# Kernel optimization log

Measured on AMD Instinct MI355X. Metric: run time of the kernel, lower is better.

Reference implementation:

```python
import jax, jax.numpy as jnp
import numpy as np

N = 20000   # total_nodes
B = 8       # batch of graphs
E = 320000  # edges per graph (avg degree 16)
FD = 128    # node feature dim
D = 64      # latent_dim
H = 128     # mlp_hidden
MAX_LV = 2  # message-passing levels


def setup_inputs() -> dict:
    key = jax.random.key(0)
    ks = jax.random.split(key, 16)
    def gn(k, shape, fan_in):
        return jax.random.normal(k, shape, dtype=jnp.float32) / np.sqrt(fan_in)
    edges_src = jax.random.randint(ks[0], (B, E), 0, N)
    edges_dst = jax.random.randint(ks[1], (B, E), 0, N)
    # row-normalized adjacency weights: w = 1/deg(dst)  (GraphNormTool mean norm)
    deg = jax.vmap(lambda d: jnp.zeros((N,), jnp.float32).at[d].add(1.0))(edges_dst)
    edge_w = 1.0 / jnp.take_along_axis(deg, edges_dst, axis=1)
    return {
        "node_features": jax.random.normal(ks[2], (N, FD), dtype=jnp.float32),
        "w_n2l": gn(ks[3], (FD, D), FD),
        "bias_n2l": jnp.zeros((D,), jnp.float32),
        "bias_picked": gn(ks[4], (1, D), D),
        "conv_W": gn(ks[5], (D, D), D),
        "conv_b": jnp.zeros((D,), jnp.float32),
        "lin1_W": gn(ks[6], (2 * D, H), 2 * D),
        "lin1_b": jnp.zeros((H,), jnp.float32),
        "lout_W": gn(ks[7], (H, D), H),
        "lout_b": jnp.zeros((D,), jnp.float32),
        "edge_w": edge_w,
        "edges_src": edges_src,
        "edges_dst": edges_dst,
        "target_nodes": jax.random.randint(ks[8], (B,), 0, N),
        "picked_nodes": jax.random.randint(ks[9], (B,), 0, N),
    }


def reference(node_features, w_n2l, bias_n2l, bias_picked, conv_W, conv_b,
              lin1_W, lin1_b, lout_W, lout_b, edge_w,
              edges_src, edges_dst, target_nodes, picked_nodes):
    # shared input linear: [N, D]
    base = node_features @ w_n2l + bias_n2l

    def per_graph(src, dst, w, tgt, picked):
        # inject picked-node bias (sparse one-hot spmm in original)
        input_message = base.at[picked].add(bias_picked[0])
        h = jax.nn.relu(input_message)
        for _ in range(MAX_LV):
            # n2npool = adj @ h  (sparse spmm via gather + segment_sum)
            pooled = jax.ops.segment_sum(h[src] * w[:, None], dst, num_segments=N)
            h = jax.nn.relu(pooled @ conv_W + conv_b + input_message)
        target_embed = h[tgt]                      # [D]
        graph_embed = jnp.mean(h, axis=0)          # [D]
        e = jnp.concatenate([h, jnp.broadcast_to(graph_embed, (N, D))], axis=1)
        e = jax.nn.relu(e @ lin1_W + lin1_b)       # [N, H]
        raw = e @ lout_W + lout_b                  # [N, D]
        return raw @ target_embed                  # bilin_q: [N]

    q = jax.vmap(per_graph)(edges_src, edges_dst, edge_w, target_nodes, picked_nodes)
    return q  # [B, N] per-node Q values per graph
```

## Files before the change

kernel.cpp:

```cpp
#include <hip/hip_runtime.h>
#include <hip/hip_bf16.h>
#include <hip/hip_fp16.h>

#define Nn 20000
#define NR 20001
#define Bg 8
#define Eg 320000
#define FDim 128
#define Dd 64
#define Hh 128
#define NCH 16
#define CHE (Eg / NCH)

typedef _Float16 v2h __attribute__((ext_vector_type(2)));
typedef unsigned short u16;

__device__ __forceinline__ float bcastf(float v, int l) {
  return __int_as_float(__builtin_amdgcn_readlane(__float_as_int(v), l));
}
__device__ __forceinline__ int bcasti(int v, int l) {
  return __builtin_amdgcn_readlane(v, l);
}
__device__ __forceinline__ v2h u2h2(unsigned u) { return __builtin_bit_cast(v2h, u); }
__device__ __forceinline__ unsigned h22u(__half2 h) { return __builtin_bit_cast(unsigned, h); }
__device__ __forceinline__ float fdot2f(v2h a, v2h b, float c) {
  return __builtin_amdgcn_fdot2(a, b, c, false);
}

__global__ __launch_bounds__(256) void k_base(const float* __restrict__ x,
                                              const float* __restrict__ W,
                                              const float* __restrict__ b,
                                              float* __restrict__ base,
                                              __half* __restrict__ b16,
                                              __half* __restrict__ b16p) {
  __shared__ float Wl[FDim * Dd];
  int t = threadIdx.x;
  for (int i = t; i < FDim * Dd; i += 256) Wl[i] = W[i];
  __syncthreads();
  int wv = t >> 6, lane = t & 63;
  float bias = b[lane];
  for (int row = blockIdx.x * 4 + wv; row < NR; row += gridDim.x * 4) {
    if (row == Nn) {
      b16[(size_t)row * Dd + lane] = __float2half(0.f);
      continue;
    }
    float x0 = x[row * FDim + lane];
    float x1 = x[row * FDim + 64 + lane];
    float acc = bias;
#pragma unroll
    for (int k = 0; k < 64; ++k) acc = fmaf(bcastf(x0, k), Wl[k * Dd + lane], acc);
#pragma unroll
    for (int k = 0; k < 64; ++k) acc = fmaf(bcastf(x1, k), Wl[(64 + k) * Dd + lane], acc);
    base[row * Dd + lane] = acc;
    b16[row * Dd + lane] = __float2half(fmaxf(acc, 0.f));
    b16p[row * Dd + lane] = __float2half(acc);
  }
}

__global__ __launch_bounds__(1024) void k_hist(const int* __restrict__ dst,
                                               int* __restrict__ hpart) {
  __shared__ int lh[Nn];
  int g = blockIdx.x & 7;
  int c = blockIdx.x >> 3;
  for (int i = threadIdx.x; i < Nn; i += 1024) lh[i] = 0;
  __syncthreads();
  const int* dp = dst + (size_t)g * Eg + c * CHE;
  for (int e4 = threadIdx.x * 4; e4 < CHE; e4 += 4096) {
    int4 d4 = *(const int4*)(dp + e4);
    atomicAdd(&lh[d4.x], 1);
    atomicAdd(&lh[d4.y], 1);
    atomicAdd(&lh[d4.z], 1);
    atomicAdd(&lh[d4.w], 1);
  }
  __syncthreads();
  int* out = hpart + (size_t)(g * NCH + c) * Nn;
  for (int i = threadIdx.x; i < Nn; i += 1024) out[i] = lh[i];
}

__global__ __launch_bounds__(1024) void k_scan(int* __restrict__ hpart,
                                               int* __restrict__ deg,
                                               int* __restrict__ offs,
                                               __half* __restrict__ hA) {
  int g = blockIdx.x;
  if (threadIdx.x < Dd)
    hA[((size_t)g * NR + Nn) * Dd + threadIdx.x] = __float2half(0.f);
  int* hp = hpart + (size_t)g * NCH * Nn;
  int* dp = deg + g * Nn;
  int* op = offs + g * Nn;
  __shared__ int wsum[16];
  __shared__ int carrysh;
  if (threadIdx.x == 0) carrysh = 0;
  int lane = threadIdx.x & 63, wv = threadIdx.x >> 6;
  __syncthreads();
  for (int b0 = 0; b0 < Nn; b0 += 4096) {
    int gidx = b0 + threadIdx.x * 4;
    bool ok = (gidx < Nn);
    int4 s = make_int4(0, 0, 0, 0);
    if (ok) {
#pragma unroll
      for (int c = 0; c < NCH; ++c) {
        int4 v = *(const int4*)(hp + (size_t)c * Nn + gidx);
        s.x += v.x; s.y += v.y; s.z += v.z; s.w += v.w;
      }
      *(int4*)(dp + gidx) = s;
    }
    int s0 = s.x, s1 = s0 + s.y, s2 = s1 + s.z, s3 = s2 + s.w;
    int incl = s3;
#pragma unroll
    for (int off = 1; off < 64; off <<= 1) {
      int y = __shfl_up(incl, off, 64);
      if (lane >= off) incl += y;
    }
    if (lane == 63) wsum[wv] = incl;
    __syncthreads();
    if (threadIdx.x < 16) {
      int w = wsum[threadIdx.x];
      int wincl = w;
#pragma unroll
      for (int off = 1; off < 16; off <<= 1) {
        int y = __shfl_up(wincl, off, 64);
        if (lane >= off) wincl += y;
      }
      wsum[threadIdx.x] = wincl - w;
    }
    __syncthreads();
    int cc = carrysh;
    int excl = cc + wsum[wv] + incl - s3;
    if (ok) {
      int4 o;
      o.x = excl; o.y = excl + s0; o.z = excl + s1; o.w = excl + s2;
      *(int4*)(op + gidx) = o;
      int4 run = o;
#pragma unroll
      for (int c = 0; c < NCH; ++c) {
        int4 v = *(const int4*)(hp + (size_t)c * Nn + gidx);
        *(int4*)(hp + (size_t)c * Nn + gidx) = run;
        run.x += v.x; run.y += v.y; run.z += v.z; run.w += v.w;
      }
    }
    __syncthreads();
    if (threadIdx.x == 1023) carrysh = cc + wsum[15] + __shfl(incl, 63, 64);
    __syncthreads();
  }
}

__global__ __launch_bounds__(1024) void k_scatter(const int* __restrict__ src,
                                                  const int* __restrict__ dst,
                                                  const int* __restrict__ basep,
                                                  u16* __restrict__ ssrc) {
  __shared__ int lc[Nn];
  int g = blockIdx.x & 7;
  int c = blockIdx.x >> 3;
  for (int i = threadIdx.x; i < Nn; i += 1024) lc[i] = 0;
  __syncthreads();
  const int* dp = dst + (size_t)g * Eg + c * CHE;
  const int* sp_in = src + (size_t)g * Eg + c * CHE;
  const int* bp = basep + (size_t)(g * NCH + c) * Nn;
  u16* out = ssrc + (size_t)g * Eg;
  for (int e4 = threadIdx.x * 4; e4 < CHE; e4 += 4096) {
    int4 d4 = *(const int4*)(dp + e4);
    int4 s4 = *(const int4*)(sp_in + e4);
    int r0 = atomicAdd(&lc[d4.x], 1); out[bp[d4.x] + r0] = (u16)s4.x;
    int r1 = atomicAdd(&lc[d4.y], 1); out[bp[d4.y] + r1] = (u16)s4.y;
    int r2 = atomicAdd(&lc[d4.z], 1); out[bp[d4.z] + r2] = (u16)s4.z;
    int r3 = atomicAdd(&lc[d4.w], 1); out[bp[d4.w] + r3] = (u16)s4.w;
  }
}

template <bool LV1>
__global__ __launch_bounds__(256, 4) void k_level(
    const __half* __restrict__ gsrc,
    __half* __restrict__ hout,
    const float* __restrict__ base,
    const __half* __restrict__ b16p,
    const float* __restrict__ convW, const float* __restrict__ convb,
    const float* __restrict__ biasp, const int* __restrict__ picked,
    const int* __restrict__ deg, const int* __restrict__ offs,
    const u16* __restrict__ ssrc, float* __restrict__ gsum) {
  int t = threadIdx.x;
  int wv = t >> 6, lane = t & 63;
  unsigned wc[32];
#pragma unroll
  for (int d2 = 0; d2 < 32; ++d2)
    wc[d2] = h22u(__floats2half2_rn(convW[(2 * d2) * Dd + lane],
                                    (convW[(2 * d2 + 1) * Dd + lane])));
#pragma unroll
  for (int d2 = 0; d2 < 32; ++d2) asm volatile("" : "+v"(wc[d2]));
  float cb = convb[lane];
  float bp = biasp[lane];
  int g = blockIdx.x & 7;
  int lb = blockIdx.x >> 3;
  int pstride = (gridDim.x >> 3) * 4;
  int pick = picked[g];
  int gN = g * Nn;
  const u16* sp = ssrc + (size_t)g * Eg;
  const __half* hsrc = LV1 ? gsrc : (gsrc + (size_t)g * NR * Dd);
  __half* outp = LV1 ? (hout + (size_t)g * NR * Dd) : (hout + (size_t)g * Nn * Dd);
  float delta = 0.f;
  if (LV1) {
    float db = base[(size_t)pick * Dd + lane];
    float d16 = __half2float(__float2half(fmaxf(db, 0.f)));
    delta = fmaxf(db + bp, 0.f) - d16;
  }
  float gs = 0.f;

  for (int p = lb * 4 + wv; p < Nn / 2; p += pstride) {
    int i0 = p * 2, i1 = i0 + 1;
    int2 dg2 = *(const int2*)&deg[gN + i0];
    int d0 = dg2.x, dtot = d0 + dg2.y;
    int beg0 = offs[gN + i0];

    float a0 = 0.f, aT = 0.f;
    if (dtot <= 64) {
      int svm = Nn;
      if (lane < dtot) svm = (int)sp[beg0 + lane];
      if (LV1) {
        unsigned long long pm = __ballot(svm == pick);
        unsigned long long m0 = (d0 >= 64) ? ~0ull : ((1ull << d0) - 1ull);
        a0 += (float)__popcll(pm & m0) * delta;
        aT += (float)__popcll(pm) * delta;
      }
      int nch = (dtot + 7) >> 3;
      for (int c = 0; c < nch; ++c) {
        int j = c * 8;
        int s0 = bcasti(svm, j + 0), s1 = bcasti(svm, j + 1);
        int s2 = bcasti(svm, j + 2), s3 = bcasti(svm, j + 3);
        int s4 = bcasti(svm, j + 4), s5 = bcasti(svm, j + 5);
        int s6 = bcasti(svm, j + 6), s7 = bcasti(svm, j + 7);
        float v0 = __half2float(hsrc[((unsigned)s0 << 6) + lane]);
        float v1 = __half2float(hsrc[((unsigned)s1 << 6) + lane]);
        float v2 = __half2float(hsrc[((unsigned)s2 << 6) + lane]);
        float v3 = __half2float(hsrc[((unsigned)s3 << 6) + lane]);
        float v4 = __half2float(hsrc[((unsigned)s4 << 6) + lane]);
        float v5 = __half2float(hsrc[((unsigned)s5 << 6) + lane]);
        float v6 = __half2float(hsrc[((unsigned)s6 << 6) + lane]);
        float v7 = __half2float(hsrc[((unsigned)s7 << 6) + lane]);
        float cs = ((v0 + v1) + (v2 + v3)) + ((v4 + v5) + (v6 + v7));
        aT += cs;
        if (j + 8 <= d0) {
          a0 += cs;
        } else if (j < d0) {
          int r = d0 - j;
          float pfx = (r > 0 ? v0 : 0.f) + (r > 1 ? v1 : 0.f) + (r > 2 ? v2 : 0.f) +
                      (r > 3 ? v3 : 0.f) + (r > 4 ? v4 : 0.f) + (r > 5 ? v5 : 0.f) +
                      (r > 6 ? v6 : 0.f);
          a0 += pfx;
        }
      }
    } else {
      int c0cnt = 0, cTcnt = 0;
      int end0 = beg0 + d0, end1 = beg0 + dtot;
      for (int e = beg0; e < end0; ++e) {
        int s = (int)sp[e];
        if (LV1) c0cnt += (s == pick);
        a0 += __half2float(hsrc[((unsigned)s << 6) + lane]);
      }
      aT = a0;
      for (int e = end0; e < end1; ++e) {
        int s = (int)sp[e];
        if (LV1) cTcnt += (s == pick);
        aT += __half2float(hsrc[((unsigned)s << 6) + lane]);
      }
      if (LV1) {
        a0 += (float)c0cnt * delta;
        aT += (float)(cTcnt + c0cnt) * delta;
      }
    }
    float a1 = aT - a0;
    float acc0 = a0 * (d0 ? 1.0f / (float)d0 : 0.f);
    float acc1 = a1 * (dg2.y ? 1.0f / (float)dg2.y : 0.f);

    unsigned p0 = h22u(__floats2half2_rn(acc0, __shfl_down(acc0, 1, 64)));
    unsigned p1 = h22u(__floats2half2_rn(acc1, __shfl_down(acc1, 1, 64)));

    float o0a = __half2float(b16p[(size_t)i0 * Dd + lane]) + cb, o0b = 0.f;
    float o1a = __half2float(b16p[(size_t)i1 * Dd + lane]) + cb, o1b = 0.f;
    if (i0 == pick) o0a += bp;
    if (i1 == pick) o1a += bp;
#pragma unroll
    for (int d2 = 0; d2 < 32; d2 += 2) {
      v2h m00 = u2h2(bcasti(p0, 2 * d2)),     m01 = u2h2(bcasti(p0, 2 * d2 + 2));
      v2h m10 = u2h2(bcasti(p1, 2 * d2)),     m11 = u2h2(bcasti(p1, 2 * d2 + 2));
      o0a = fdot2f(m00, u2h2(wc[d2]), o0a);
      o0b = fdot2f(m01, u2h2(wc[d2 + 1]), o0b);
      o1a = fdot2f(m10, u2h2(wc[d2]), o1a);
      o1b = fdot2f(m11, u2h2(wc[d2 + 1]), o1b);
    }
    float out0 = fmaxf(o0a + o0b, 0.f);
    float out1 = fmaxf(o1a + o1b, 0.f);
    outp[(size_t)i0 * Dd + lane] = __float2half(out0);
    outp[(size_t)i1 * Dd + lane] = __float2half(out1);
    if (!LV1) gs += out0 + out1;
  }
  if (!LV1) atomicAdd(&gsum[g * Dd + lane], gs);
}

__global__ __launch_bounds__(128) void k_prep(
    const __half* __restrict__ h2, const float* __restrict__ gsum,
    const int* __restrict__ tgt, const float* __restrict__ lin1W,
    const float* __restrict__ lin1b, const float* __restrict__ loutW,
    const float* __restrict__ loutb, float* __restrict__ cvec,
    float* __restrict__ uvec, float* __restrict__ cscal) {
  int g = blockIdx.x;
  int k = threadIdx.x;
  __shared__ float tv[Dd], ge[Dd];
  if (k < Dd) {
    tv[k] = __half2float(h2[(size_t)g * Nn * Dd + (size_t)tgt[g] * Dd + k]);
    ge[k] = gsum[g * Dd + k] * (1.0f / Nn);
  }
  __syncthreads();
  float cv = lin1b[k];
#pragma unroll 8
  for (int d = 0; d < Dd; ++d) cv = fmaf(ge[d], lin1W[(Dd + d) * Hh + k], cv);
  cvec[g * Hh + k] = cv;
  float uu = 0.f;
#pragma unroll 8
  for (int j = 0; j < Dd; ++j) uu = fmaf(loutW[k * Dd + j], tv[j], uu);
  uvec[g * Hh + k] = uu;
  if (k == 0) {
    float c = 0.f;
    for (int j = 0; j < Dd; ++j) c += loutb[j] * tv[j];
    cscal[g] = c;
  }
}

__global__ __launch_bounds__(256) void k_final(
    const __half* __restrict__ h2, const float* __restrict__ lin1W,
    const float* __restrict__ cvec, const float* __restrict__ uvec,
    const float* __restrict__ cscal, float* __restrict__ out) {
  __shared__ unsigned Wl2[32 * Hh];
  int t = threadIdx.x;
  for (int i = t; i < 32 * Hh; i += 256) {
    int d2 = i >> 7, c = i & 127;
    Wl2[i] = h22u(__floats2half2_rn(lin1W[(2 * d2) * Hh + c],
                                    lin1W[(2 * d2 + 1) * Hh + c]));
  }
  __syncthreads();
  int wv = t >> 6, lane = t & 63;
  int lr = lane & 31, hi = lane >> 5;
  int tot = Bg * Nn / 4;
  for (int p = blockIdx.x * 4 + wv; p < tot; p += gridDim.x * 4) {
    int row0 = p * 4;
    int g = row0 / Nn;
    int i0 = row0 - g * Nn;
    const __half2* hb = (const __half2*)(h2 + (size_t)g * Nn * Dd);
    unsigned ra = h22u(hb[(size_t)(i0 + hi) * 32 + lr]);
    unsigned rb = h22u(hb[(size_t)(i0 + 2 + hi) * 32 + lr]);
    float c0 = cvec[g * Hh + lane], c1 = cvec[g * Hh + 64 + lane];
    float u0 = uvec[g * Hh + lane], u1 = uvec[g * Hh + 64 + lane];
    float za0 = c0, za1 = c1, zb0 = c0, zb1 = c1;
    float zc0 = c0, zc1 = c1, zd0 = c0, zd1 = c1;
#pragma unroll
    for (int d2 = 0; d2 < 32; ++d2) {
      v2h w0 = u2h2(Wl2[d2 * Hh + lane]);
      v2h w1 = u2h2(Wl2[d2 * Hh + 64 + lane]);
      v2h a0 = u2h2(bcasti(ra, d2)), a1 = u2h2(bcasti(ra, 32 + d2));
      v2h b0 = u2h2(bcasti(rb, d2)), b1 = u2h2(bcasti(rb, 32 + d2));
      za0 = fdot2f(a0, w0, za0);  za1 = fdot2f(a0, w1, za1);
      zb0 = fdot2f(a1, w0, zb0);  zb1 = fdot2f(a1, w1, zb1);
      zc0 = fdot2f(b0, w0, zc0);  zc1 = fdot2f(b0, w1, zc1);
      zd0 = fdot2f(b1, w0, zd0);  zd1 = fdot2f(b1, w1, zd1);
    }
    float s0 = fmaxf(za0, 0.f) * u0 + fmaxf(za1, 0.f) * u1;
    float s1 = fmaxf(zb0, 0.f) * u0 + fmaxf(zb1, 0.f) * u1;
    float s2 = fmaxf(zc0, 0.f) * u0 + fmaxf(zc1, 0.f) * u1;
    float s3 = fmaxf(zd0, 0.f) * u0 + fmaxf(zd1, 0.f) * u1;
#pragma unroll
    for (int off = 32; off; off >>= 1) {
      s0 += __shfl_xor(s0, off, 64);
      s1 += __shfl_xor(s1, off, 64);
      s2 += __shfl_xor(s2, off, 64);
      s3 += __shfl_xor(s3, off, 64);
    }
    if (lane == 0) {
      float cc = cscal[g];
      out[row0] = s0 + cc;
      out[row0 + 1] = s1 + cc;
      out[row0 + 2] = s2 + cc;
      out[row0 + 3] = s3 + cc;
    }
  }
}

extern "C" void kernel_launch(void* const* d_in, const int* in_sizes, int n_in,
                              void* d_out, int out_size, void* d_ws, size_t ws_size,
                              hipStream_t stream) {
  const float* node_features = (const float*)d_in[0];
  const float* w_n2l        = (const float*)d_in[1];
  const float* bias_n2l     = (const float*)d_in[2];
  const float* bias_picked  = (const float*)d_in[3];
  const float* conv_W       = (const float*)d_in[4];
  const float* conv_b       = (const float*)d_in[5];
  const float* lin1_W       = (const float*)d_in[6];
  const float* lin1_b       = (const float*)d_in[7];
  const float* lout_W       = (const float*)d_in[8];
  const float* lout_b       = (const float*)d_in[9];
  const int*   edges_src    = (const int*)d_in[11];
  const int*   edges_dst    = (const int*)d_in[12];
  const int*   target_nodes = (const int*)d_in[13];
  const int*   picked_nodes = (const int*)d_in[14];
  float* q_out = (float*)d_out;

  float*  base  = (float*)d_ws;
  __half* b16   = (__half*)(base + (size_t)Nn * Dd);
  __half* b16p  = b16 + (size_t)NR * Dd;
  __half* hAh   = b16p + (size_t)Nn * Dd;
  __half* h2    = hAh + (size_t)Bg * NR * Dd;
  int*    deg   = (int*)(h2 + (size_t)Bg * Nn * Dd);
  float*  gsum  = (float*)(deg + (size_t)Bg * Nn);
  int*    offs  = (int*)(gsum + Bg * Dd);
  int*    hpart = offs + (size_t)Bg * Nn;
  u16*    ssrc  = (u16*)(hpart + (size_t)Bg * NCH * Nn);
  float*  cvec  = (float*)(ssrc + (size_t)Bg * Eg);
  float*  uvec  = cvec + Bg * Hh;
  float*  csc   = uvec + Bg * Hh;

  hipMemsetAsync(gsum, 0, (size_t)Bg * Dd * sizeof(float), stream);

  k_base<<<512, 256, 0, stream>>>(node_features, w_n2l, bias_n2l, base, b16, b16p);
  k_hist<<<NCH * Bg, 1024, 0, stream>>>(edges_dst, hpart);
  k_scan<<<Bg, 1024, 0, stream>>>(hpart, deg, offs, hAh);
  k_scatter<<<NCH * Bg, 1024, 0, stream>>>(edges_src, edges_dst, hpart, ssrc);
  k_level<true><<<2048, 256, 0, stream>>>(b16, hAh, base, b16p, conv_W, conv_b,
                                          bias_picked, picked_nodes, deg, offs,
                                          ssrc, gsum);
  k_level<false><<<2048, 256, 0, stream>>>(hAh, h2, base, b16p, conv_W, conv_b,
                                           bias_picked, picked_nodes, deg, offs,
                                           ssrc, gsum);
  k_prep<<<Bg, 128, 0, stream>>>(h2, gsum, target_nodes, lin1_W, lin1_b, lout_W,
                                 lout_b, cvec, uvec, csc);
  k_final<<<2048, 256, 0, stream>>>(h2, lin1_W, cvec, uvec, csc, q_out);
}
```

Baseline: 406.8 us.

## Vectorize neighbor gathers with 16-byte loads and move conv weights to LDS

The level kernel's neighbor aggregation now has each 8-lane subgroup fetch a full half-precision row with one 16-byte load. Eight edges are processed per wave step, then reduced with xor shuffles and packed into half2 for the conv matmul, replacing eight scalar per-lane half loads per chunk. Conv weights move from 32 pinned registers to shared memory, which frees registers but adds LDS reads inside the inner dot loop. The base linear also switches to fp16 dot2 over half-packed inputs and weights, which lowers precision of the base activations.

Result: no change. 407.8 us (+0.2%).

```diff
diff --git a/kernel.cpp b/kernel.cpp
--- a/kernel.cpp
+++ b/kernel.cpp
@@ -13,6 +13,7 @@
 #define CHE (Eg / NCH)
 
 typedef _Float16 v2h __attribute__((ext_vector_type(2)));
+typedef float v2f __attribute__((ext_vector_type(2)));
 typedef unsigned short u16;
 
 __device__ __forceinline__ float bcastf(float v, int l) {
@@ -23,6 +24,10 @@
 }
 __device__ __forceinline__ v2h u2h2(unsigned u) { return __builtin_bit_cast(v2h, u); }
 __device__ __forceinline__ unsigned h22u(__half2 h) { return __builtin_bit_cast(unsigned, h); }
+__device__ __forceinline__ unsigned pkrtz(float a, float b) {
+  auto r = __builtin_amdgcn_cvt_pkrtz(a, b);
+  return __builtin_bit_cast(unsigned, r);
+}
 __device__ __forceinline__ float fdot2f(v2h a, v2h b, float c) {
   return __builtin_amdgcn_fdot2(a, b, c, false);
 }
@@ -33,9 +38,12 @@
                                               float* __restrict__ base,
                                               __half* __restrict__ b16,
                                               __half* __restrict__ b16p) {
-  __shared__ float Wl[FDim * Dd];
+  __shared__ unsigned Wl2[64 * Dd];
   int t = threadIdx.x;
-  for (int i = t; i < FDim * Dd; i += 256) Wl[i] = W[i];
+  for (int i = t; i < 64 * Dd; i += 256) {
+    int k = i >> 6, o = i & 63;
+    Wl2[i] = pkrtz(W[(2 * k) * Dd + o], W[(2 * k + 1) * Dd + o]);
+  }
   __syncthreads();
   int wv = t >> 6, lane = t & 63;
   float bias = b[lane];
@@ -44,16 +52,18 @@
       b16[(size_t)row * Dd + lane] = __float2half(0.f);
       continue;
     }
-    float x0 = x[row * FDim + lane];
-    float x1 = x[row * FDim + 64 + lane];
-    float acc = bias;
-#pragma unroll
-    for (int k = 0; k < 64; ++k) acc = fmaf(bcastf(x0, k), Wl[k * Dd + lane], acc);
-#pragma unroll
-    for (int k = 0; k < 64; ++k) acc = fmaf(bcastf(x1, k), Wl[(64 + k) * Dd + lane], acc);
-    base[row * Dd + lane] = acc;
-    b16[row * Dd + lane] = __float2half(fmaxf(acc, 0.f));
-    b16p[row * Dd + lane] = __float2half(acc);
+    float2 xf = *(const float2*)&x[(size_t)row * FDim + lane * 2];
+    unsigned xh = pkrtz(xf.x, xf.y);
+    float acc = bias, acc2 = 0.f;
+#pragma unroll
+    for (int k = 0; k < 64; k += 2) {
+      acc = fdot2f(u2h2(bcasti(xh, k)), u2h2(Wl2[k * Dd + lane]), acc);
+      acc2 = fdot2f(u2h2(bcasti(xh, k + 1)), u2h2(Wl2[(k + 1) * Dd + lane]), acc2);
+    }
+    acc += acc2;
+    base[(size_t)row * Dd + lane] = acc;
+    b16[(size_t)row * Dd + lane] = __float2half(fmaxf(acc, 0.f));
+    b16p[(size_t)row * Dd + lane] = __float2half(acc);
   }
 }
 
@@ -177,15 +187,14 @@
     const float* __restrict__ biasp, const int* __restrict__ picked,
     const int* __restrict__ deg, const int* __restrict__ offs,
     const u16* __restrict__ ssrc, float* __restrict__ gsum) {
+  __shared__ unsigned Wl2[32 * Dd];
   int t = threadIdx.x;
+  for (int i = t; i < 32 * Dd; i += 256) {
+    int k = i >> 6, o = i & 63;
+    Wl2[i] = pkrtz(convW[(2 * k) * Dd + o], convW[(2 * k + 1) * Dd + o]);
+  }
+  __syncthreads();
   int wv = t >> 6, lane = t & 63;
-  unsigned wc[32];
-#pragma unroll
-  for (int d2 = 0; d2 < 32; ++d2)
-    wc[d2] = h22u(__floats2half2_rn(convW[(2 * d2) * Dd + lane],
-                                    (convW[(2 * d2 + 1) * Dd + lane])));
-#pragma unroll
-  for (int d2 = 0; d2 < 32; ++d2) asm volatile("" : "+v"(wc[d2]));
   float cb = convb[lane];
   float bp = biasp[lane];
   int g = blockIdx.x & 7;
@@ -196,95 +205,117 @@
   const u16* sp = ssrc + (size_t)g * Eg;
   const __half* hsrc = LV1 ? gsrc : (gsrc + (size_t)g * NR * Dd);
   __half* outp = LV1 ? (hout + (size_t)g * NR * Dd) : (hout + (size_t)g * Nn * Dd);
-  float delta = 0.f;
+  int sub = lane >> 3;
+  int grp8 = (lane & 7) << 3;
+  v2f dpk[4] = {v2f{0.f, 0.f}, v2f{0.f, 0.f}, v2f{0.f, 0.f}, v2f{0.f, 0.f}};
   if (LV1) {
     float db = base[(size_t)pick * Dd + lane];
     float d16 = __half2float(__float2half(fmaxf(db, 0.f)));
-    delta = fmaxf(db + bp, 0.f) - d16;
+    float delta = fmaxf(db + bp, 0.f) - d16;
+#pragma unroll
+    for (int r = 0; r < 4; ++r) {
+      dpk[r].x = __shfl(delta, grp8 + 2 * r, 64);
+      dpk[r].y = __shfl(delta, grp8 + 2 * r + 1, 64);
+    }
   }
   float gs = 0.f;
 
   for (int p = lb * 4 + wv; p < Nn / 2; p += pstride) {
     int i0 = p * 2, i1 = i0 + 1;
     int2 dg2 = *(const int2*)&deg[gN + i0];
-    int d0 = dg2.x, dtot = d0 + dg2.y;
+    int d0 = dg2.x, d1 = dg2.y, dtot = d0 + d1;
     int beg0 = offs[gN + i0];
-
-    float a0 = 0.f, aT = 0.f;
+    unsigned pk0[4], pk1[4];
+
     if (dtot <= 64) {
       int svm = Nn;
       if (lane < dtot) svm = (int)sp[beg0 + lane];
+      int cnt0 = 0, cnt1 = 0;
       if (LV1) {
         unsigned long long pm = __ballot(svm == pick);
         unsigned long long m0 = (d0 >= 64) ? ~0ull : ((1ull << d0) - 1ull);
-        a0 += (float)__popcll(pm & m0) * delta;
-        aT += (float)__popcll(pm) * delta;
-      }
-      int nch = (dtot + 7) >> 3;
-      for (int c = 0; c < nch; ++c) {
-        int j = c * 8;
-        int s0 = bcasti(svm, j + 0), s1 = bcasti(svm, j + 1);
-        int s2 = bcasti(svm, j + 2), s3 = bcasti(svm, j + 3);
-        int s4 = bcasti(svm, j + 4), s5 = bcasti(svm, j + 5);
-        int s6 = bcasti(svm, j + 6), s7 = bcasti(svm, j + 7);
-        float v0 = __half2float(hsrc[((unsigned)s0 << 6) + lane]);
-        float v1 = __half2float(hsrc[((unsigned)s1 << 6) + lane]);
-        float v2 = __half2float(hsrc[((unsigned)s2 << 6) + lane]);
-        float v3 = __half2float(hsrc[((unsigned)s3 << 6) + lane]);
-        float v4 = __half2float(hsrc[((unsigned)s4 << 6) + lane]);
-        float v5 = __half2float(hsrc[((unsigned)s5 << 6) + lane]);
-        float v6 = __half2float(hsrc[((unsigned)s6 << 6) + lane]);
-        float v7 = __half2float(hsrc[((unsigned)s7 << 6) + lane]);
-        float cs = ((v0 + v1) + (v2 + v3)) + ((v4 + v5) + (v6 + v7));
-        aT += cs;
-        if (j + 8 <= d0) {
-          a0 += cs;
-        } else if (j < d0) {
-          int r = d0 - j;
-          float pfx = (r > 0 ? v0 : 0.f) + (r > 1 ? v1 : 0.f) + (r > 2 ? v2 : 0.f) +
-                      (r > 3 ? v3 : 0.f) + (r > 4 ? v4 : 0.f) + (r > 5 ? v5 : 0.f) +
-                      (r > 6 ? v6 : 0.f);
-          a0 += pfx;
+        cnt0 = __popcll(pm & m0);
+        cnt1 = __popcll(pm) - cnt0;
+      }
+      auto ROWSUM = [&](int jb, int d, int cnt, unsigned* pk) {
+        v2f a0 = {0.f, 0.f}, a1 = {0.f, 0.f}, a2 = {0.f, 0.f}, a3 = {0.f, 0.f};
+        for (int j = 0; j < d; j += 8) {
+          int e = j + sub;
+          int s = __shfl(svm, jb + e, 64);
+          s = (e < d) ? s : Nn;
+          uint4 u = *(const uint4*)(hsrc + (((unsigned)s) << 6) + grp8);
+          v2h q0 = u2h2(u.x), q1 = u2h2(u.y), q2 = u2h2(u.z), q3 = u2h2(u.w);
+          a0 += (v2f){(float)q0.x, (float)q0.y};
+          a1 += (v2f){(float)q1.x, (float)q1.y};
+          a2 += (v2f){(float)q2.x, (float)q2.y};
+          a3 += (v2f){(float)q3.x, (float)q3.y};
         }
-      }
+#pragma unroll
+        for (int off = 8; off <= 32; off <<= 1) {
+          a0 += (v2f){__shfl_xor(a0.x, off, 64), __shfl_xor(a0.y, off, 64)};
+          a1 += (v2f){__shfl_xor(a1.x, off, 64), __shfl_xor(a1.y, off, 64)};
+          a2 += (v2f){__shfl_xor(a2.x, off, 64), __shfl_xor(a2.y, off, 64)};
+          a3 += (v2f){__shfl_xor(a3.x, off, 64), __shfl_xor(a3.y, off, 64)};
+        }
+        if (LV1) {
+          float c = (float)cnt;
+          a0 += c * dpk[0]; a1 += c * dpk[1]; a2 += c * dpk[2]; a3 += c * dpk[3];
+        }
+        float ws = d ? 1.0f / (float)d : 0.f;
+        a0 *= ws; a1 *= ws; a2 *= ws; a3 *= ws;
+        pk[0] = pkrtz(a0.x, a0.y);
+        pk[1] = pkrtz(a1.x, a1.y);
+        pk[2] = pkrtz(a2.x, a2.y);
+        pk[3] = pkrtz(a3.x, a3.y);
+      };
+      ROWSUM(0, d0, cnt0, pk0);
+      ROWSUM(d0, d1, cnt1, pk1);
     } else {
-      int c0cnt = 0, cTcnt = 0;
+      float acc0 = 0.f, acc1 = 0.f;
+      int c0cnt = 0, c1cnt = 0;
       int end0 = beg0 + d0, end1 = beg0 + dtot;
       for (int e = beg0; e < end0; ++e) {
         int s = (int)sp[e];
         if (LV1) c0cnt += (s == pick);
-        a0 += __half2float(hsrc[((unsigned)s << 6) + lane]);
-      }
-      aT = a0;
+        acc0 += __half2float(hsrc[((unsigned)s << 6) + lane]);
+      }
       for (int e = end0; e < end1; ++e) {
         int s = (int)sp[e];
-        if (LV1) cTcnt += (s == pick);
-        aT += __half2float(hsrc[((unsigned)s << 6) + lane]);
+        if (LV1) c1cnt += (s == pick);
+        acc1 += __half2float(hsrc[((unsigned)s << 6) + lane]);
       }
       if (LV1) {
-        a0 += (float)c0cnt * delta;
-        aT += (float)(cTcnt + c0cnt) * delta;
-      }
-    }
-    float a1 = aT - a0;
-    float acc0 = a0 * (d0 ? 1.0f / (float)d0 : 0.f);
-    float acc1 = a1 * (dg2.y ? 1.0f / (float)dg2.y : 0.f);
-
-    unsigned p0 = h22u(__floats2half2_rn(acc0, __shfl_down(acc0, 1, 64)));
-    unsigned p1 = h22u(__floats2half2_rn(acc1, __shfl_down(acc1, 1, 64)));
+        float db = base[(size_t)pick * Dd + lane];
+        float d16 = __half2float(__float2half(fmaxf(db, 0.f)));
+        float delta = fmaxf(db + bp, 0.f) - d16;
+        acc0 += (float)c0cnt * delta;
+        acc1 += (float)c1cnt * delta;
+      }
+      acc0 *= (d0 ? 1.0f / (float)d0 : 0.f);
+      acc1 *= (d1 ? 1.0f / (float)d1 : 0.f);
+#pragma unroll
+      for (int r = 0; r < 4; ++r) {
+        pk0[r] = pkrtz(__shfl(acc0, grp8 + 2 * r, 64), __shfl(acc0, grp8 + 2 * r + 1, 64));
+        pk1[r] = pkrtz(__shfl(acc1, grp8 + 2 * r, 64), __shfl(acc1, grp8 + 2 * r + 1, 64));
+      }
+    }
 
     float o0a = __half2float(b16p[(size_t)i0 * Dd + lane]) + cb, o0b = 0.f;
     float o1a = __half2float(b16p[(size_t)i1 * Dd + lane]) + cb, o1b = 0.f;
     if (i0 == pick) o0a += bp;
     if (i1 == pick) o1a += bp;
 #pragma unroll
-    for (int d2 = 0; d2 < 32; d2 += 2) {
-      v2h m00 = u2h2(bcasti(p0, 2 * d2)),     m01 = u2h2(bcasti(p0, 2 * d2 + 2));
-      v2h m10 = u2h2(bcasti(p1, 2 * d2)),     m11 = u2h2(bcasti(p1, 2 * d2 + 2));
-      o0a = fdot2f(m00, u2h2(wc[d2]), o0a);
-      o0b = fdot2f(m01, u2h2(wc[d2 + 1]), o0b);
-      o1a = fdot2f(m10, u2h2(wc[d2]), o1a);
-      o1b = fdot2f(m11, u2h2(wc[d2 + 1]), o1b);
+    for (int k = 0; k < 32; k += 2) {
+      unsigned w0 = Wl2[k * Dd + lane];
+      unsigned w1 = Wl2[(k + 1) * Dd + lane];
+      unsigned m00 = (unsigned)bcasti((int)pk0[k & 3], k >> 2);
+      unsigned m01 = (unsigned)bcasti((int)pk0[(k + 1) & 3], (k + 1) >> 2);
+      unsigned m10 = (unsigned)bcasti((int)pk1[k & 3], k >> 2);
+      unsigned m11 = (unsigned)bcasti((int)pk1[(k + 1) & 3], (k + 1) >> 2);
+      o0a = fdot2f(u2h2(m00), u2h2(w0), o0a);
+      o0b = fdot2f(u2h2(m01), u2h2(w1), o0b);
+      o1a = fdot2f(u2h2(m10), u2h2(w0), o1a);
+      o1b = fdot2f(u2h2(m11), u2h2(w1), o1b);
     }
     float out0 = fmaxf(o0a + o0b, 0.f);
     float out1 = fmaxf(o1a + o1b, 0.f);
@@ -332,8 +363,7 @@
   int t = threadIdx.x;
   for (int i = t; i < 32 * Hh; i += 256) {
     int d2 = i >> 7, c = i & 127;
-    Wl2[i] = h22u(__floats2half2_rn(lin1W[(2 * d2) * Hh + c],
-                                    lin1W[(2 * d2 + 1) * Hh + c]));
+    Wl2[i] = pkrtz(lin1W[(2 * d2) * Hh + c], lin1W[(2 * d2 + 1) * Hh + c]);
   }
   __syncthreads();
   int wv = t >> 6, lane = t & 63;
@@ -415,7 +445,7 @@
   float*  uvec  = cvec + Bg * Hh;
   float*  csc   = uvec + Bg * Hh;
 
-  hipMemsetAsync(gsum, 0, (size_t)Bg * Dd * sizeof(float), stream);
+  (void)hipMemsetAsync(gsum, 0, (size_t)Bg * Dd * sizeof(float), stream);
 
   k_base<<<512, 256, 0, stream>>>(node_features, w_n2l, bias_n2l, base, b16, b16p);
   k_hist<<<NCH * Bg, 1024, 0, stream>>>(edges_dst, hpart);
```
